# Optimization experiments

Hardware: AMD Instinct MI355X
Metric: run time of the kernel (lower is better)

## Reference

```python
import jax, jax.numpy as jnp
import numpy as np

B, C, N = 8, 64, 4096

def setup_inputs() -> dict:
    key = jax.random.key(0)
    k1, k2, k3 = jax.random.split(key, 3)
    k = jax.random.normal(k1, (B, C, N), dtype=jnp.float32)
    q = jax.random.normal(k2, (B, C, N), dtype=jnp.float32)
    v = jax.random.normal(k3, (B, C, N), dtype=jnpp.float32) if False else jax.random.normal(k3, (B, C, N), dtype=jnp.float32)
    return {"k": k, "q": q, "v": v}

def reference(k, q, v):
    input_dim = k.shape[1]  # C
    # similarity = k^T @ q : [B, N, N]
    scores = jnp.einsum('bcn,bcm->bnm', k, q) / jnp.sqrt(jnp.float32(input_dim))
    attn = jax.nn.softmax(scores, axis=-1)  # softmax over last dim (query positions m)
    # out = attn @ v^T : [B, N, C], then transpose back to [B, C, N]
    out = jnp.einsum('bnm,bcm->bcn', attn, v)
    return out
```

## Files before the change

kernel.cpp:

```cpp
#include <hip/hip_runtime.h>
#include <stdint.h>

typedef __attribute__((ext_vector_type(8)))  __bf16        bf16x8;
typedef __attribute__((ext_vector_type(8)))  unsigned short u16x8;
typedef __attribute__((ext_vector_type(4)))  float          f32x4;
typedef __attribute__((ext_vector_type(16))) float          f32x16;
typedef __attribute__((ext_vector_type(4)))  unsigned int   u32x4;

#define NB 8
#define NC 64
#define NN 4096
#define NCHUNK 64
#define CHUNK_U16 4096
#define SPLITQ 4

#define EXP2F(x) __builtin_amdgcn_exp2f(x)

__device__ __forceinline__ unsigned short f2bf(float x) {
    unsigned int u = __builtin_bit_cast(unsigned int, x);
    u += 0x7fffu + ((u >> 16) & 1u);
    return (unsigned short)(u >> 16);
}
__device__ __forceinline__ unsigned int pk2(float a, float b) {
    unsigned short x = __builtin_bit_cast(unsigned short, (__bf16)a);
    unsigned short y = __builtin_bit_cast(unsigned short, (__bf16)b);
    return (unsigned int)x | ((unsigned int)y << 16);
}

__global__ __launch_bounds__(256) void prepass(
    const float* __restrict__ qp, const float* __restrict__ vp,
    unsigned short* __restrict__ qfo, unsigned short* __restrict__ vfo)
{
    __shared__ float lt[64][68];
    const int orig = blockIdx.x;
    const int bid = (orig & 7) * 64 + (orig >> 3);
    const int b = bid >> 6, mc = bid & 63;
    const int m0 = mc * 64;
    const int tid = threadIdx.x;
    const float* qb = qp + (size_t)b * NC * NN;
    const float* vb = vp + (size_t)b * NC * NN;
    unsigned short* qfc = qfo + (size_t)bid * CHUNK_U16;
    unsigned short* vfc = vfo + (size_t)bid * CHUNK_U16;

    #pragma unroll
    for (int rep = 0; rep < 4; ++rep) {
        int idx = tid + 256 * rep;
        int c = idx >> 4, m4 = (idx & 15) << 2;
        f32x4 xv = *reinterpret_cast<const f32x4*>(qb + (size_t)c * NN + m0 + m4);
        lt[m4+0][c] = xv[0]; lt[m4+1][c] = xv[1];
        lt[m4+2][c] = xv[2]; lt[m4+3][c] = xv[3];
    }
    __syncthreads();
    #pragma unroll
    for (int rep = 0; rep < 2; ++rep) {
        int fid = tid + 256 * rep;
        int l = fid & 63, kk = (fid >> 6) & 3, mt = fid >> 8;
        int m = 32 * mt + (l & 31), c0 = 16 * kk + 8 * (l >> 5);
        u16x8 ov;
        #pragma unroll
        for (int e = 0; e < 8; ++e) ov[e] = f2bf(lt[m][c0 + e]);
        *reinterpret_cast<u16x8*>(qfc + (size_t)fid * 8) = ov;
    }
    __syncthreads();
    #pragma unroll
    for (int rep = 0; rep < 4; ++rep) {
        int idx = tid + 256 * rep;
        int c = idx >> 4, m4 = (idx & 15) << 2;
        f32x4 xv = *reinterpret_cast<const f32x4*>(vb + (size_t)c * NN + m0 + m4);
        *reinterpret_cast<f32x4*>(&lt[c][m4]) = xv;
    }
    __syncthreads();
    #pragma unroll
    for (int rep = 0; rep < 2; ++rep) {
        int fid = tid + 256 * rep;
        int l = fid & 63, kt = (fid >> 6) & 3, ct = fid >> 8;
        int c = 32 * ct + (l & 31), mm = 16 * kt + 8 * (l >> 5);
        u16x8 ov;
        #pragma unroll
        for (int e = 0; e < 8; ++e) ov[e] = f2bf(lt[c][mm + e]);
        *reinterpret_cast<u16x8*>(vfc + (size_t)fid * 8) = ov;
    }
}

template<int SPLITQ_T>
__global__ __launch_bounds__(256, 3) void attn10(
    const float* __restrict__ kp,
    const unsigned short* __restrict__ qfo,
    const unsigned short* __restrict__ vfo,
    float* __restrict__ part, float* __restrict__ lp)
{
    constexpr int CPQ_T = NCHUNK / SPLITQ_T;
    constexpr int TG = NN / 128;
    constexpr int PER_XCD = SPLITQ_T * TG;

    const int orig = blockIdx.x;
    const int bid  = (orig & 7) * PER_XCD + (orig >> 3);
    const int b    = bid / PER_XCD;
    const int rest = bid % PER_XCD;
    const int qid  = rest / TG;
    const int tg   = rest % TG;
    const int bn0  = tg * 128;
    const int tid = threadIdx.x;
    const int w = tid >> 6, l = tid & 63;
    const int lo5 = l & 31, hi = l >> 5;
    const int nrow = bn0 + 32 * w + lo5;

    const float kscale = 0.125f * 1.44269504088896f;
    const float* kb = kp + (size_t)b * NC * NN;
    bf16x8 kf[4];
    #pragma unroll
    for (int kk = 0; kk < 4; ++kk) {
        u16x8 t;
        #pragma unroll
        for (int e = 0; e < 8; ++e)
            t[e] = __builtin_bit_cast(unsigned short,
                      (__bf16)(kscale * kb[(size_t)(16 * kk + 8 * hi + e) * NN + nrow]));
        kf[kk] = __builtin_bit_cast(bf16x8, t);
    }

    const unsigned short* qg = qfo + (size_t)(b * NCHUNK + qid * CPQ_T) * CHUNK_U16;
    const unsigned short* vg = vfo + (size_t)(b * NCHUNK + qid * CPQ_T) * CHUNK_U16;

    f32x16 zro;
    #pragma unroll
    for (int r = 0; r < 16; ++r) zro[r] = 0.f;
    f32x16 o0 = zro, o1 = zro;
    float sum = 0.f;

    for (int mcr = 0; mcr < CPQ_T; ++mcr) {
        const unsigned short* qc = qg + (size_t)mcr * CHUNK_U16;
        const unsigned short* vc = vg + (size_t)mcr * CHUNK_U16;

        u16x8 a[8];
        #pragma unroll
        for (int f = 0; f < 8; ++f)
            a[f] = *reinterpret_cast<const u16x8*>(qc + (f * 64 + l) * 8);

        __builtin_amdgcn_s_setprio(1);
        f32x16 s0 = __builtin_amdgcn_mfma_f32_32x32x16_bf16(__builtin_bit_cast(bf16x8, a[0]), kf[0], zro, 0, 0, 0);
        f32x16 s1 = __builtin_amdgcn_mfma_f32_32x32x16_bf16(__builtin_bit_cast(bf16x8, a[4]), kf[0], zro, 0, 0, 0);
        #pragma unroll
        for (int kk = 1; kk < 4; ++kk) {
            s0 = __builtin_amdgcn_mfma_f32_32x32x16_bf16(__builtin_bit_cast(bf16x8, a[kk]),     kf[kk], s0, 0, 0, 0);
            s1 = __builtin_amdgcn_mfma_f32_32x32x16_bf16(__builtin_bit_cast(bf16x8, a[4 + kk]), kf[kk], s1, 0, 0, 0);
        }
        __builtin_amdgcn_s_setprio(0);

        u16x8 vf[8];
        #pragma unroll
        for (int f = 0; f < 8; ++f)
            vf[f] = *reinterpret_cast<const u16x8*>(vc + (f * 64 + l) * 8);

        float ps0 = 0.f, ps1 = 0.f, ps2 = 0.f, ps3 = 0.f;
        #pragma unroll
        for (int r = 0; r < 16; r += 4) {
            s0[r]   = EXP2F(s0[r]);   ps0 += s0[r];
            s0[r+1] = EXP2F(s0[r+1]); ps1 += s0[r+1];
            s0[r+2] = EXP2F(s0[r+2]); ps2 += s0[r+2];
            s0[r+3] = EXP2F(s0[r+3]); ps3 += s0[r+3];
        }
        #pragma unroll
        for (int r = 0; r < 16; r += 4) {
            s1[r]   = EXP2F(s1[r]);   ps0 += s1[r];
            s1[r+1] = EXP2F(s1[r+1]); ps1 += s1[r+1];
            s1[r+2] = EXP2F(s1[r+2]); ps2 += s1[r+2];
            s1[r+3] = EXP2F(s1[r+3]); ps3 += s1[r+3];
        }
        sum += (ps0 + ps1) + (ps2 + ps3);

        #pragma unroll
        for (int kt = 0; kt < 4; ++kt) {
            const f32x16& sm = (kt < 2) ? s0 : s1;
            const int qA = 2 * (kt & 1);
            unsigned int w0 = pk2(sm[4*qA+0], sm[4*qA+1]);
            unsigned int w1 = pk2(sm[4*qA+2], sm[4*qA+3]);
            unsigned int w2 = pk2(sm[4*qA+4], sm[4*qA+5]);
            unsigned int w3 = pk2(sm[4*qA+6], sm[4*qA+7]);
            asm volatile("v_permlane32_swap_b32 %0, %1" : "+v"(w0), "+v"(w2));
            asm volatile("v_permlane32_swap_b32 %0, %1" : "+v"(w1), "+v"(w3));
            u32x4 pf = (u32x4){w0, w1, w2, w3};
            bf16x8 pB = __builtin_bit_cast(bf16x8, pf);
            __builtin_amdgcn_s_setprio(1);
            o0 = __builtin_amdgcn_mfma_f32_32x32x16_bf16(__builtin_bit_cast(bf16x8, vf[kt]),     pB, o0, 0, 0, 0);
            o1 = __builtin_amdgcn_mfma_f32_32x32x16_bf16(__builtin_bit_cast(bf16x8, vf[4 + kt]), pB, o1, 0, 0, 0);
            __builtin_amdgcn_s_setprio(0);
        }
    }

    sum += (float)__shfl_xor(sum, 32);
    const int t64 = (bn0 >> 6) + (w >> 1);
    const int rowoff = 32 * (w & 1);
    const int pidx = (b * 64 + t64) * SPLITQ_T + qid;
    float* po = part + (size_t)pidx * 4096;
    #pragma unroll
    for (int r = 0; r < 16; ++r) {
        int cb = (r & 3) + 8 * (r >> 2) + 4 * hi;
        po[cb * 64 + rowoff + lo5]        = o0[r];
        po[(32 + cb) * 64 + rowoff + lo5] = o1[r];
    }
    if (hi == 0) lp[(size_t)pidx * 64 + rowoff + lo5] = sum;
}

__global__ __launch_bounds__(256) void combine2(
    const float* __restrict__ part, const float* __restrict__ lp,
    float* __restrict__ outp, int splitq)
{
    __shared__ float sinv[64];
    const int orig = blockIdx.x;
    const int bid = (orig & 7) * 64 + (orig >> 3);
    const int b = bid >> 6, tile = bid & 63;
    const int n0 = tile * 64;
    const int t = threadIdx.x;
    const int pb = bid * splitq;

    if (t < 64) {
        float L = 0.f;
        for (int q = 0; q < splitq; ++q) L += lp[(size_t)(pb + q) * 64 + t];
        sinv[t] = 1.0f / L;
    }
    __syncthreads();

    float* ob = outp + (size_t)b * NC * NN;
    #pragma unroll
    for (int it = 0; it < 4; ++it) {
        int idx = it * 1024 + t * 4;
        int ch = idx >> 6, r0 = idx & 63;
        f32x4 acc = (f32x4){0.f, 0.f, 0.f, 0.f};
        for (int q = 0; q < splitq; ++q) {
            f32x4 v = *reinterpret_cast<const f32x4*>(part + (size_t)(pb + q) * 4096 + idx);
            acc += v;
        }
        f32x4 res;
        #pragma unroll
        for (int u = 0; u < 4; ++u) res[u] = acc[u] * sinv[r0 + u];
        *reinterpret_cast<f32x4*>(ob + (size_t)ch * NN + n0 + r0) = res;
    }
}

__global__ __launch_bounds__(128) void attn2(
    const float* __restrict__ kp,
    const unsigned short* __restrict__ qfo,
    const unsigned short* __restrict__ vfo,
    float* __restrict__ outp)
{
    __shared__ unsigned short sb[2][2 * CHUNK_U16];
    const int orig = blockIdx.x;
    const int bid  = (orig & 7) * 64 + (orig >> 3);
    const int b = bid >> 6, nt = bid & 63;
    const int n0 = nt * 64;
    const int tid = threadIdx.x;
    const int w = tid >> 6, l = tid & 63;
    const int lo5 = l & 31, hi = l >> 5;
    const int nrow = n0 + 32 * w + lo5;
    const float kscale = 0.125f * 1.44269504088896f;
    const float* kb = kp + (size_t)b * NC * NN;
    bf16x8 kf[4];
    #pragma unroll
    for (int kk = 0; kk < 4; ++kk) {
        u16x8 t;
        #pragma unroll
        for (int e = 0; e < 8; ++e)
            t[e] = f2bf(kscale * kb[(size_t)(16 * kk + 8 * hi + e) * NN + nrow]);
        kf[kk] = __builtin_bit_cast(bf16x8, t);
    }
    const unsigned short* qg = qfo + (size_t)(b * 64) * CHUNK_U16;
    const unsigned short* vg = vfo + (size_t)(b * 64) * CHUNK_U16;
    auto stage = [&](int mc, int buf) {
        const unsigned short* gq = qg + (size_t)mc * CHUNK_U16;
        const unsigned short* gv = vg + (size_t)mc * CHUNK_U16;
        #pragma unroll
        for (int i = 0; i < 4; ++i) {
            int seg = w * 4 + i;
            int off = seg * 512 + l * 8;
            __builtin_amdgcn_global_load_lds(
                (const __attribute__((address_space(1))) void*)(gq + off),
                (__attribute__((address_space(3))) void*)(&sb[buf][seg * 512]), 16, 0, 0);
            __builtin_amdgcn_global_load_lds(
                (const __attribute__((address_space(1))) void*)(gv + off),
                (__attribute__((address_space(3))) void*)(&sb[buf][CHUNK_U16 + seg * 512]), 16, 0, 0);
        }
    };
    stage(0, 0);
    __syncthreads();
    f32x16 o0, o1;
    #pragma unroll
    for (int r = 0; r < 16; ++r) { o0[r] = 0.f; o1[r] = 0.f; }
    float m_run = -1e30f, l_run = 0.f;
    for (int mc = 0; mc < NCHUNK; ++mc) {
        const int cur = mc & 1;
        if (mc + 1 < NCHUNK) stage(mc + 1, cur ^ 1);
        const unsigned short* qb_ = &sb[cur][0];
        const unsigned short* vb_ = &sb[cur][CHUNK_U16];
        f32x16 s0, s1;
        #pragma unroll
        for (int r = 0; r < 16; ++r) { s0[r] = 0.f; s1[r] = 0.f; }
        #pragma unroll
        for (int kk = 0; kk < 4; ++kk) {
            u16x8 a0 = *reinterpret_cast<const u16x8*>(qb_ + ((0 * 4 + kk) * 64 + l) * 8);
            u16x8 a1 = *reinterpret_cast<const u16x8*>(qb_ + ((1 * 4 + kk) * 64 + l) * 8);
            s0 = __builtin_amdgcn_mfma_f32_32x32x16_bf16(__builtin_bit_cast(bf16x8, a0), kf[kk], s0, 0, 0, 0);
            s1 = __builtin_amdgcn_mfma_f32_32x32x16_bf16(__builtin_bit_cast(bf16x8, a1), kf[kk], s1, 0, 0, 0);
        }
        float pmax = s0[0];
        #pragma unroll
        for (int r = 1; r < 16; ++r) pmax = fmaxf(pmax, s0[r]);
        #pragma unroll
        for (int r = 0; r < 16; ++r) pmax = fmaxf(pmax, s1[r]);
        pmax = fmaxf(pmax, (float)__shfl_xor(pmax, 32));
        const float mn = fmaxf(m_run, pmax);
        const float alpha = EXP2F(m_run - mn);
        float sum = 0.f;
        #pragma unroll
        for (int r = 0; r < 16; ++r) { s0[r] = EXP2F(s0[r] - mn); sum += s0[r]; }
        #pragma unroll
        for (int r = 0; r < 16; ++r) { s1[r] = EXP2F(s1[r] - mn); sum += s1[r]; }
        sum += (float)__shfl_xor(sum, 32);
        l_run = l_run * alpha + sum;
        m_run = mn;
        #pragma unroll
        for (int r = 0; r < 16; ++r) { o0[r] *= alpha; o1[r] *= alpha; }
        #pragma unroll
        for (int kt = 0; kt < 4; ++kt) {
            const f32x16& sm = (kt < 2) ? s0 : s1;
            const int qA = 2 * (kt & 1);
            unsigned int dA0 = pk2(sm[4 * qA + 0], sm[4 * qA + 1]);
            unsigned int dA1 = pk2(sm[4 * qA + 2], sm[4 * qA + 3]);
            unsigned int dB0 = pk2(sm[4 * qA + 4], sm[4 * qA + 5]);
            unsigned int dB1 = pk2(sm[4 * qA + 6], sm[4 * qA + 7]);
            unsigned int sA0 = (unsigned int)__shfl_xor((int)dA0, 32);
            unsigned int sA1 = (unsigned int)__shfl_xor((int)dA1, 32);
            unsigned int sB0 = (unsigned int)__shfl_xor((int)dB0, 32);
            unsigned int sB1 = (unsigned int)__shfl_xor((int)dB1, 32);
            u32x4 pf;
            if (hi == 0) pf = (u32x4){dA0, dA1, sA0, sA1};
            else         pf = (u32x4){sB0, sB1, dB0, dB1};
            bf16x8 pB = __builtin_bit_cast(bf16x8, pf);
            u16x8 v0 = *reinterpret_cast<const u16x8*>(vb_ + ((0 * 4 + kt) * 64 + l) * 8);
            u16x8 v1 = *reinterpret_cast<const u16x8*>(vb_ + ((1 * 4 + kt) * 64 + l) * 8);
            o0 = __builtin_amdgcn_mfma_f32_32x32x16_bf16(__builtin_bit_cast(bf16x8, v0), pB, o0, 0, 0, 0);
            o1 = __builtin_amdgcn_mfma_f32_32x32x16_bf16(__builtin_bit_cast(bf16x8, v1), pB, o1, 0, 0, 0);
        }
        __syncthreads();
    }
    const float inv = 1.0f / l_run;
    float* ob = outp + (size_t)b * NC * NN;
    #pragma unroll
    for (int r = 0; r < 16; ++r) {
        int cb = (r & 3) + 8 * (r >> 2) + 4 * hi;
        ob[(size_t)cb * NN + n0 + 32 * w + lo5]        = o0[r] * inv;
        ob[(size_t)(32 + cb) * NN + n0 + 32 * w + lo5] = o1[r] * inv;
    }
}

__global__ __launch_bounds__(256) void attn_fwd(
    const float* __restrict__ kp, const float* __restrict__ qp,
    const float* __restrict__ vp, float* __restrict__ outp)
{
    __shared__ unsigned short qs[8][64][8];
    __shared__ unsigned short vs[8][64][8];
    __shared__ unsigned short ps[4][2][64][8];
    const int orig = blockIdx.x;
    const int bid  = (orig & 7) * 64 + (orig >> 3);
    const int b  = bid >> 6;
    const int n0 = (bid & 63) * 64;
    const int tid = threadIdx.x;
    const int w = tid >> 6, l = tid & 63, g = l >> 4, j = l & 15;
    const float* kb = kp + (size_t)b * NC * NN;
    const float* qb = qp + (size_t)b * NC * NN;
    const float* vb = vp + (size_t)b * NC * NN;
    bf16x8 ak[2];
    #pragma unroll
    for (int kk = 0; kk < 2; ++kk) {
        u16x8 tmp;
        #pragma unroll
        for (int e = 0; e < 8; ++e)
            tmp[e] = f2bf(kb[(size_t)(32*kk + 8*g + e) * NN + (n0 + 16*w + j)]);
        ak[kk] = __builtin_bit_cast(bf16x8, tmp);
    }
    f32x4 o[4];
    float m_run[4], l_run[4];
    #pragma unroll
    for (int ct = 0; ct < 4; ++ct) o[ct] = (f32x4){0.f,0.f,0.f,0.f};
    #pragma unroll
    for (int r = 0; r < 4; ++r) { m_run[r] = -1e30f; l_run[r] = 0.0f; }
    for (int m0 = 0; m0 < NN; m0 += 64) {
        __syncthreads();
        #pragma unroll
        for (int it = 0; it < 4; ++it) {
            int f = tid + 256*it;
            int c = f >> 4, m4 = (f & 15) << 2;
            f32x4 qv = *reinterpret_cast<const f32x4*>(qb + (size_t)c*NN + m0 + m4);
            f32x4 vv = *reinterpret_cast<const f32x4*>(vb + (size_t)c*NN + m0 + m4);
            int kkq = c >> 5, eq = c & 7, gq = (c >> 3) & 3, tq = m4 >> 4;
            #pragma unroll
            for (int u = 0; u < 4; ++u)
                qs[kkq*4 + tq][16*gq + ((m4 + u) & 15)][eq] = f2bf(qv[u]);
            int ctv = c >> 4, jv = c & 15, kkv = m4 >> 5, gv = (m4 >> 3) & 3, ev = m4 & 7;
            #pragma unroll
            for (int u = 0; u < 4; ++u)
                vs[kkv*4 + ctv][16*gv + jv][ev + u] = f2bf(vv[u]);
        }
        __syncthreads();
        f32x4 s[4];
        #pragma unroll
        for (int t = 0; t < 4; ++t) {
            f32x4 acc = (f32x4){0.f,0.f,0.f,0.f};
            #pragma unroll
            for (int kk = 0; kk < 2; ++kk) {
                u16x8 raw = *reinterpret_cast<const u16x8*>(&qs[kk*4 + t][l][0]);
                acc = __builtin_amdgcn_mfma_f32_16x16x32_bf16(ak[kk], __builtin_bit_cast(bf16x8, raw), acc, 0,0,0);
            }
            s[t] = acc * 0.125f;
        }
        float alpha[4];
        #pragma unroll
        for (int r = 0; r < 4; ++r) {
            float m1 = fmaxf(fmaxf(s[0][r], s[1][r]), fmaxf(s[2][r], s[3][r]));
            #pragma unroll
            for (int off = 1; off < 16; off <<= 1) m1 = fmaxf(m1, __shfl_xor(m1, off));
            float mn = fmaxf(m_run[r], m1);
            alpha[r] = __expf(m_run[r] - mn);
            m_run[r] = mn;
            float acc = 0.0f;
            #pragma unroll
            for (int t = 0; t < 4; ++t) { float p = __expf(s[t][r] - mn); s[t][r] = p; acc += p; }
            #pragma unroll
            for (int off = 1; off < 16; off <<= 1) acc += __shfl_xor(acc, off);
            l_run[r] = l_run[r] * alpha[r] + acc;
        }
        {
            int srcl = (j >> 2) << 4;
            float a0 = __shfl(alpha[0], srcl), a1 = __shfl(alpha[1], srcl);
            float a2 = __shfl(alpha[2], srcl), a3 = __shfl(alpha[3], srcl);
            int rs = j & 3;
            float ac = (rs==0)?a0:(rs==1)?a1:(rs==2)?a2:a3;
            #pragma unroll
            for (int ct = 0; ct < 4; ++ct) o[ct] *= ac;
        }
        #pragma unroll
        for (int t = 0; t < 4; ++t) {
            int m = 16*t + j;
            #pragma unroll
            for (int r = 0; r < 4; ++r)
                ps[w][m >> 5][((m >> 3) & 3)*16 + 4*g + r][m & 7] = f2bf(s[t][r]);
        }
        asm volatile("s_waitcnt lgkmcnt(0)" ::: "memory");
        #pragma unroll
        for (int kk2 = 0; kk2 < 2; ++kk2) {
            u16x8 rp = *reinterpret_cast<const u16x8*>(&ps[w][kk2][l][0]);
            bf16x8 bp = __builtin_bit_cast(bf16x8, rp);
            #pragma unroll
            for (int ct = 0; ct < 4; ++ct) {
                u16x8 rv = *reinterpret_cast<const u16x8*>(&vs[kk2*4 + ct][l][0]);
                o[ct] = __builtin_amdgcn_mfma_f32_16x16x32_bf16(__builtin_bit_cast(bf16x8, rv), bp, o[ct], 0,0,0);
            }
        }
    }
    {
        int srcl = (j >> 2) << 4;
        float l0 = __shfl(l_run[0], srcl), l1 = __shfl(l_run[1], srcl);
        float l2 = __shfl(l_run[2], srcl), l3 = __shfl(l_run[3], srcl);
        int rs = j & 3;
        float lc = (rs==0)?l0:(rs==1)?l1:(rs==2)?l2:l3;
        float inv = 1.0f / lc;
        #pragma unroll
        for (int ct = 0; ct < 4; ++ct)
            #pragma unroll
            for (int r = 0; r < 4; ++r)
                outp[(size_t)b*NC*NN + (size_t)(16*ct + 4*g + r)*NN + (n0 + 16*w + j)] = o[ct][r] * inv;
    }
}

extern "C" void kernel_launch(void* const* d_in, const int* in_sizes, int n_in,
                              void* d_out, int out_size, void* d_ws, size_t ws_size,
                              hipStream_t stream) {
    const float* kp = (const float*)d_in[0];
    const float* qp = (const float*)d_in[1];
    const float* vp = (const float*)d_in[2];
    float* op = (float*)d_out;
    const size_t FRAG_BYTES = (size_t)2 * NB * NCHUNK * CHUNK_U16 * sizeof(unsigned short);
    unsigned short* qfo = (unsigned short*)d_ws;
    unsigned short* vfo = qfo + (size_t)NB * NCHUNK * CHUNK_U16;

    const size_t NEED = FRAG_BYTES
        + (size_t)NB * 64 * SPLITQ * 4096 * sizeof(float)
        + (size_t)NB * 64 * SPLITQ * 64 * sizeof(float);

    if (ws_size >= NEED) {
        float* part = (float*)((char*)d_ws + FRAG_BYTES);
        float* lpp  = part + (size_t)NB * 64 * SPLITQ * 4096;
        hipLaunchKernelGGL(prepass, dim3(NB * NCHUNK), dim3(256), 0, stream, qp, vp, qfo, vfo);
        hipLaunchKernelGGL(attn10<SPLITQ>, dim3(NB * SPLITQ * (NN / 128)), dim3(256), 0, stream,
                           kp, qfo, vfo, part, lpp);
        hipLaunchKernelGGL(combine2, dim3(NB * 64), dim3(256), 0, stream, part, lpp, op, SPLITQ);
    } else if (ws_size >= FRAG_BYTES) {
        hipLaunchKernelGGL(prepass, dim3(NB * NCHUNK), dim3(256), 0, stream, qp, vp, qfo, vfo);
        hipLaunchKernelGGL(attn2, dim3(NB * NCHUNK), dim3(128), 0, stream, kp, qfo, vfo, op);
    } else {
        hipLaunchKernelGGL(attn_fwd, dim3(512), dim3(256), 0, stream, kp, qp, vp, op);
    }
}
```

Measured before the change: 67.90 us.

## Use single-wave attention blocks with split-8 over queries and earlier V loads

```diff
diff --git a/kernel.cpp b/kernel.cpp
--- a/kernel.cpp
+++ b/kernel.cpp
@@ -12,7 +12,6 @@
 #define NN 4096
 #define NCHUNK 64
 #define CHUNK_U16 4096
-#define SPLITQ 4
 
 #define EXP2F(x) __builtin_amdgcn_exp2f(x)
 
@@ -83,27 +82,26 @@
 }
 
 template<int SPLITQ_T>
-__global__ __launch_bounds__(256, 3) void attn10(
+__global__ __launch_bounds__(64, 3) void attn11(
     const float* __restrict__ kp,
     const unsigned short* __restrict__ qfo,
     const unsigned short* __restrict__ vfo,
     float* __restrict__ part, float* __restrict__ lp)
 {
     constexpr int CPQ_T = NCHUNK / SPLITQ_T;
-    constexpr int TG = NN / 128;
-    constexpr int PER_XCD = SPLITQ_T * TG;
+    constexpr int NT32 = NN / 32;
+    constexpr int PER_XCD = SPLITQ_T * NT32;
 
     const int orig = blockIdx.x;
     const int bid  = (orig & 7) * PER_XCD + (orig >> 3);
     const int b    = bid / PER_XCD;
     const int rest = bid % PER_XCD;
-    const int qid  = rest / TG;
-    const int tg   = rest % TG;
-    const int bn0  = tg * 128;
-    const int tid = threadIdx.x;
-    const int w = tid >> 6, l = tid & 63;
+    const int qid  = rest / NT32;
+    const int t32  = rest % NT32;
+    const int n0 = t32 * 32;
+    const int l = threadIdx.x;
     const int lo5 = l & 31, hi = l >> 5;
-    const int nrow = bn0 + 32 * w + lo5;
+    const int nrow = n0 + lo5;
 
     const float kscale = 0.125f * 1.44269504088896f;
     const float* kb = kp + (size_t)b * NC * NN;
@@ -135,6 +133,10 @@
         #pragma unroll
         for (int f = 0; f < 8; ++f)
             a[f] = *reinterpret_cast<const u16x8*>(qc + (f * 64 + l) * 8);
+        u16x8 vf[8];
+        #pragma unroll
+        for (int f = 0; f < 8; ++f)
+            vf[f] = *reinterpret_cast<const u16x8*>(vc + (f * 64 + l) * 8);
 
         __builtin_amdgcn_s_setprio(1);
         f32x16 s0 = __builtin_amdgcn_mfma_f32_32x32x16_bf16(__builtin_bit_cast(bf16x8, a[0]), kf[0], zro, 0, 0, 0);
@@ -145,11 +147,6 @@
             s1 = __builtin_amdgcn_mfma_f32_32x32x16_bf16(__builtin_bit_cast(bf16x8, a[4 + kk]), kf[kk], s1, 0, 0, 0);
         }
         __builtin_amdgcn_s_setprio(0);
-
-        u16x8 vf[8];
-        #pragma unroll
-        for (int f = 0; f < 8; ++f)
-            vf[f] = *reinterpret_cast<const u16x8*>(vc + (f * 64 + l) * 8);
 
         float ps0 = 0.f, ps1 = 0.f, ps2 = 0.f, ps3 = 0.f;
         #pragma unroll
@@ -188,8 +185,8 @@
     }
 
     sum += (float)__shfl_xor(sum, 32);
-    const int t64 = (bn0 >> 6) + (w >> 1);
-    const int rowoff = 32 * (w & 1);
+    const int t64 = t32 >> 1;
+    const int rowoff = 32 * (t32 & 1);
     const int pidx = (b * 64 + t64) * SPLITQ_T + qid;
     float* po = part + (size_t)pidx * 4096;
     #pragma unroll
@@ -482,17 +479,27 @@
     unsigned short* qfo = (unsigned short*)d_ws;
     unsigned short* vfo = qfo + (size_t)NB * NCHUNK * CHUNK_U16;
 
-    const size_t NEED = FRAG_BYTES
-        + (size_t)NB * 64 * SPLITQ * 4096 * sizeof(float)
-        + (size_t)NB * 64 * SPLITQ * 64 * sizeof(float);
-
-    if (ws_size >= NEED) {
+    auto need = [&](int splitq) {
+        return FRAG_BYTES
+             + (size_t)NB * 64 * splitq * 4096 * sizeof(float)
+             + (size_t)NB * 64 * splitq * 64 * sizeof(float);
+    };
+
+    int splitq = 0;
+    if      (ws_size >= need(8)) splitq = 8;
+    else if (ws_size >= need(4)) splitq = 4;
+
+    if (splitq) {
         float* part = (float*)((char*)d_ws + FRAG_BYTES);
-        float* lpp  = part + (size_t)NB * 64 * SPLITQ * 4096;
+        float* lpp  = part + (size_t)NB * 64 * splitq * 4096;
         hipLaunchKernelGGL(prepass, dim3(NB * NCHUNK), dim3(256), 0, stream, qp, vp, qfo, vfo);
-        hipLaunchKernelGGL(attn10<SPLITQ>, dim3(NB * SPLITQ * (NN / 128)), dim3(256), 0, stream,
-                           kp, qfo, vfo, part, lpp);
-        hipLaunchKernelGGL(combine2, dim3(NB * 64), dim3(256), 0, stream, part, lpp, op, SPLITQ);
+        if (splitq == 8)
+            hipLaunchKernelGGL(attn11<8>, dim3(NB * 8 * (NN / 32)), dim3(64), 0, stream,
+                               kp, qfo, vfo, part, lpp);
+        else
+            hipLaunchKernelGGL(attn11<4>, dim3(NB * 4 * (NN / 32)), dim3(64), 0, stream,
+                               kp, qfo, vfo, part, lpp);
+        hipLaunchKernelGGL(combine2, dim3(NB * 64), dim3(256), 0, stream, part, lpp, op, splitq);
     } else if (ws_size >= FRAG_BYTES) {
         hipLaunchKernelGGL(prepass, dim3(NB * NCHUNK), dim3(256), 0, stream, qp, vp, qfo, vfo);
         hipLaunchKernelGGL(attn2, dim3(NB * NCHUNK), dim3(128), 0, stream, kp, qfo, vfo, op);
```

Measured after the change: 76.22 us. 1.12x slower.

## Split attention into single-wave blocks with register prefetch and staggered start

Applied to the files above, without the earlier changes.

```diff
diff --git a/kernel.cpp b/kernel.cpp
--- a/kernel.cpp
+++ b/kernel.cpp
@@ -83,27 +83,33 @@
 }
 
 template<int SPLITQ_T>
-__global__ __launch_bounds__(256, 3) void attn10(
+__global__ __launch_bounds__(64, 3) void attn13(
     const float* __restrict__ kp,
     const unsigned short* __restrict__ qfo,
     const unsigned short* __restrict__ vfo,
     float* __restrict__ part, float* __restrict__ lp)
 {
     constexpr int CPQ_T = NCHUNK / SPLITQ_T;
-    constexpr int TG = NN / 128;
-    constexpr int PER_XCD = SPLITQ_T * TG;
+    constexpr int NT32 = NN / 32;
+    constexpr int PER_XCD = SPLITQ_T * NT32;
 
     const int orig = blockIdx.x;
     const int bid  = (orig & 7) * PER_XCD + (orig >> 3);
     const int b    = bid / PER_XCD;
     const int rest = bid % PER_XCD;
-    const int qid  = rest / TG;
-    const int tg   = rest % TG;
-    const int bn0  = tg * 128;
-    const int tid = threadIdx.x;
-    const int w = tid >> 6, l = tid & 63;
+    const int qid  = rest / NT32;
+    const int t32  = rest % NT32;
+    const int n0 = t32 * 32;
+    const int l = threadIdx.x;
     const int lo5 = l & 31, hi = l >> 5;
-    const int nrow = bn0 + 32 * w + lo5;
+    const int nrow = n0 + lo5;
+
+    switch (orig & 3) {
+        case 1: __builtin_amdgcn_s_sleep(5);  break;
+        case 2: __builtin_amdgcn_s_sleep(10); break;
+        case 3: __builtin_amdgcn_s_sleep(15); break;
+        default: break;
+    }
 
     const float kscale = 0.125f * 1.44269504088896f;
     const float* kb = kp + (size_t)b * NC * NN;
@@ -127,15 +133,15 @@
     f32x16 o0 = zro, o1 = zro;
     float sum = 0.f;
 
+    u16x8 a[8], vf[8];
+    #pragma unroll
+    for (int f = 0; f < 8; ++f)
+        a[f] = *reinterpret_cast<const u16x8*>(qg + (f * 64 + l) * 8);
+    #pragma unroll
+    for (int f = 0; f < 8; ++f)
+        vf[f] = *reinterpret_cast<const u16x8*>(vg + (f * 64 + l) * 8);
+
     for (int mcr = 0; mcr < CPQ_T; ++mcr) {
-        const unsigned short* qc = qg + (size_t)mcr * CHUNK_U16;
-        const unsigned short* vc = vg + (size_t)mcr * CHUNK_U16;
-
-        u16x8 a[8];
-        #pragma unroll
-        for (int f = 0; f < 8; ++f)
-            a[f] = *reinterpret_cast<const u16x8*>(qc + (f * 64 + l) * 8);
-
         __builtin_amdgcn_s_setprio(1);
         f32x16 s0 = __builtin_amdgcn_mfma_f32_32x32x16_bf16(__builtin_bit_cast(bf16x8, a[0]), kf[0], zro, 0, 0, 0);
         f32x16 s1 = __builtin_amdgcn_mfma_f32_32x32x16_bf16(__builtin_bit_cast(bf16x8, a[4]), kf[0], zro, 0, 0, 0);
@@ -146,10 +152,12 @@
         }
         __builtin_amdgcn_s_setprio(0);
 
-        u16x8 vf[8];
-        #pragma unroll
-        for (int f = 0; f < 8; ++f)
-            vf[f] = *reinterpret_cast<const u16x8*>(vc + (f * 64 + l) * 8);
+        if (mcr + 1 < CPQ_T) {
+            const unsigned short* qn = qg + (size_t)(mcr + 1) * CHUNK_U16;
+            #pragma unroll
+            for (int f = 0; f < 8; ++f)
+                a[f] = *reinterpret_cast<const u16x8*>(qn + (f * 64 + l) * 8);
+        }
 
         float ps0 = 0.f, ps1 = 0.f, ps2 = 0.f, ps3 = 0.f;
         #pragma unroll
@@ -185,11 +193,18 @@
             o1 = __builtin_amdgcn_mfma_f32_32x32x16_bf16(__builtin_bit_cast(bf16x8, vf[4 + kt]), pB, o1, 0, 0, 0);
             __builtin_amdgcn_s_setprio(0);
         }
+
+        if (mcr + 1 < CPQ_T) {
+            const unsigned short* vn = vg + (size_t)(mcr + 1) * CHUNK_U16;
+            #pragma unroll
+            for (int f = 0; f < 8; ++f)
+                vf[f] = *reinterpret_cast<const u16x8*>(vn + (f * 64 + l) * 8);
+        }
     }
 
     sum += (float)__shfl_xor(sum, 32);
-    const int t64 = (bn0 >> 6) + (w >> 1);
-    const int rowoff = 32 * (w & 1);
+    const int t64 = t32 >> 1;
+    const int rowoff = 32 * (t32 & 1);
     const int pidx = (b * 64 + t64) * SPLITQ_T + qid;
     float* po = part + (size_t)pidx * 4096;
     #pragma unroll
@@ -490,7 +505,7 @@
         float* part = (float*)((char*)d_ws + FRAG_BYTES);
         float* lpp  = part + (size_t)NB * 64 * SPLITQ * 4096;
         hipLaunchKernelGGL(prepass, dim3(NB * NCHUNK), dim3(256), 0, stream, qp, vp, qfo, vfo);
-        hipLaunchKernelGGL(attn10<SPLITQ>, dim3(NB * SPLITQ * (NN / 128)), dim3(256), 0, stream,
+        hipLaunchKernelGGL(attn13<SPLITQ>, dim3(NB * SPLITQ * (NN / 32)), dim3(64), 0, stream,
                            kp, qfo, vfo, part, lpp);
         hipLaunchKernelGGL(combine2, dim3(NB * 64), dim3(256), 0, stream, part, lpp, op, SPLITQ);
     } else if (ws_size >= FRAG_BYTES) {
```

Result: slower. 70.21 us (+3.4%).

## Stage Q/V fragment chunks through triple-buffered LDS with async global-to-LDS loads

Applied to the files above, without the earlier changes.

```diff
diff --git a/kernel.cpp b/kernel.cpp
--- a/kernel.cpp
+++ b/kernel.cpp
@@ -83,7 +83,7 @@
 }
 
 template<int SPLITQ_T>
-__global__ __launch_bounds__(256, 3) void attn10(
+__global__ __launch_bounds__(256, 3) void attn14(
     const float* __restrict__ kp,
     const unsigned short* __restrict__ qfo,
     const unsigned short* __restrict__ vfo,
@@ -92,6 +92,7 @@
     constexpr int CPQ_T = NCHUNK / SPLITQ_T;
     constexpr int TG = NN / 128;
     constexpr int PER_XCD = SPLITQ_T * TG;
+    __shared__ unsigned short sb[3][2 * CHUNK_U16];
 
     const int orig = blockIdx.x;
     const int bid  = (orig & 7) * PER_XCD + (orig >> 3);
@@ -121,6 +122,26 @@
     const unsigned short* qg = qfo + (size_t)(b * NCHUNK + qid * CPQ_T) * CHUNK_U16;
     const unsigned short* vg = vfo + (size_t)(b * NCHUNK + qid * CPQ_T) * CHUNK_U16;
 
+    auto stage = [&](int mcr, int buf) {
+        const unsigned short* gq = qg + (size_t)mcr * CHUNK_U16;
+        const unsigned short* gv = vg + (size_t)mcr * CHUNK_U16;
+        #pragma unroll
+        for (int j = 0; j < 2; ++j) {
+            int off = w * 1024 + j * 512 + l * 8;
+            __builtin_amdgcn_global_load_lds(
+                (const __attribute__((address_space(1))) void*)(gq + off),
+                (__attribute__((address_space(3))) void*)(&sb[buf][w * 1024 + j * 512]),
+                16, 0, 0);
+            __builtin_amdgcn_global_load_lds(
+                (const __attribute__((address_space(1))) void*)(gv + off),
+                (__attribute__((address_space(3))) void*)(&sb[buf][CHUNK_U16 + w * 1024 + j * 512]),
+                16, 0, 0);
+        }
+    };
+
+    stage(0, 0);
+    stage(1, 1);
+
     f32x16 zro;
     #pragma unroll
     for (int r = 0; r < 16; ++r) zro[r] = 0.f;
@@ -128,13 +149,23 @@
     float sum = 0.f;
 
     for (int mcr = 0; mcr < CPQ_T; ++mcr) {
-        const unsigned short* qc = qg + (size_t)mcr * CHUNK_U16;
-        const unsigned short* vc = vg + (size_t)mcr * CHUNK_U16;
-
-        u16x8 a[8];
+        const int buf = mcr % 3;
+        if (mcr == CPQ_T - 1) asm volatile("s_waitcnt vmcnt(0)" ::: "memory");
+        else                  asm volatile("s_waitcnt vmcnt(4)" ::: "memory");
+        __builtin_amdgcn_s_barrier();
+
+        if (mcr + 2 < CPQ_T) stage(mcr + 2, (mcr + 2) % 3);
+
+        const unsigned short* qb_ = &sb[buf][0];
+        const unsigned short* vb_ = &sb[buf][CHUNK_U16];
+
+        u16x8 a[8], vf[8];
         #pragma unroll
         for (int f = 0; f < 8; ++f)
-            a[f] = *reinterpret_cast<const u16x8*>(qc + (f * 64 + l) * 8);
+            a[f] = *reinterpret_cast<const u16x8*>(qb_ + (f * 64 + l) * 8);
+        #pragma unroll
+        for (int f = 0; f < 8; ++f)
+            vf[f] = *reinterpret_cast<const u16x8*>(vb_ + (f * 64 + l) * 8);
 
         __builtin_amdgcn_s_setprio(1);
         f32x16 s0 = __builtin_amdgcn_mfma_f32_32x32x16_bf16(__builtin_bit_cast(bf16x8, a[0]), kf[0], zro, 0, 0, 0);
@@ -145,11 +176,6 @@
             s1 = __builtin_amdgcn_mfma_f32_32x32x16_bf16(__builtin_bit_cast(bf16x8, a[4 + kk]), kf[kk], s1, 0, 0, 0);
         }
         __builtin_amdgcn_s_setprio(0);
-
-        u16x8 vf[8];
-        #pragma unroll
-        for (int f = 0; f < 8; ++f)
-            vf[f] = *reinterpret_cast<const u16x8*>(vc + (f * 64 + l) * 8);
 
         float ps0 = 0.f, ps1 = 0.f, ps2 = 0.f, ps3 = 0.f;
         #pragma unroll
@@ -490,7 +516,7 @@
         float* part = (float*)((char*)d_ws + FRAG_BYTES);
         float* lpp  = part + (size_t)NB * 64 * SPLITQ * 4096;
         hipLaunchKernelGGL(prepass, dim3(NB * NCHUNK), dim3(256), 0, stream, qp, vp, qfo, vfo);
-        hipLaunchKernelGGL(attn10<SPLITQ>, dim3(NB * SPLITQ * (NN / 128)), dim3(256), 0, stream,
+        hipLaunchKernelGGL(attn14<SPLITQ>, dim3(NB * SPLITQ * (NN / 128)), dim3(256), 0, stream,
                            kp, qfo, vfo, part, lpp);
         hipLaunchKernelGGL(combine2, dim3(NB * 64), dim3(256), 0, stream, part, lpp, op, SPLITQ);
     } else if (ws_size >= FRAG_BYTES) {
```

Measured after the change: 65.76 us. 3.2% less time.
